# Optimization experiments

Measured on AMD Instinct MI355X. Metric: run time of the kernel, lower is better.

Reference implementation:

```python
import jax, jax.numpy as jnp
import numpy as np


def setup_inputs() -> dict:
    key = jax.random.key(0)
    k1, k2 = jax.random.split(key)
    querry_emb = jax.random.normal(k1, (4096, 1024), dtype=jnp.float32)
    traj_emb = jax.random.normal(k2, (8192, 1024), dtype=jnp.float32)
    return {"querry_emb": querry_emb, "traj_emb": traj_emb}


def reference(querry_emb, traj_emb):
    # Cosine-similarity score: (Q K^T) / (|q| outer |k|)  -> [Nq, Nk]
    q_norm = jnp.sqrt(jnp.sum(querry_emb * querry_emb, axis=1))  # [Nq]
    k_norm = jnp.sqrt(jnp.sum(traj_emb * traj_emb, axis=1))      # [Nk]
    score = jnp.einsum('qd,kd->qk', querry_emb, traj_emb) / (q_norm[:, None] * k_norm[None, :])
    # Softmax over key axis (torch dim=1 on [Nq, Nk])
    atten = jax.nn.softmax(score, axis=1)
    # Context: weighted sum of values (traj_emb)
    context = jnp.einsum('qk,kd->qd', atten, traj_emb)
    return context
```

## Files before the change

### kernel.cpp

```cpp
#include <hip/hip_runtime.h>

#define NQ 4096
#define NK 8192
#define DIM 1024

typedef __attribute__((ext_vector_type(8))) short short8;
typedef __attribute__((ext_vector_type(4))) float floatx4;
typedef unsigned int u32;
typedef __attribute__((address_space(3))) u32 lds_u32;
typedef __attribute__((address_space(1))) const u32 glb_u32;

__device__ __forceinline__ void gload_lds16(const void* g, void* l) {
    __builtin_amdgcn_global_load_lds((glb_u32*)g, (lds_u32*)l, 16, 0, 0);
}

__device__ __forceinline__ unsigned short f32_bf16(float f) {
    unsigned int u = __float_as_uint(f);
    u += 0x7fff + ((u >> 16) & 1);
    return (unsigned short)(u >> 16);
}

__global__ void prep_q_zero(const float* __restrict__ Q,
                            unsigned short* __restrict__ Qb,
                            float* __restrict__ inv_qn,
                            float* __restrict__ lsum,
                            float* __restrict__ out_zero) {
    int wave = threadIdx.x >> 6;
    int lane = threadIdx.x & 63;
    int row  = blockIdx.x * 4 + wave;
    const float* r = Q + (size_t)row * DIM;
    float s = 0.f;
#pragma unroll
    for (int c = 0; c < 4; ++c) {
        float4 f = *(const float4*)(r + c * 256 + lane * 4);
        s += f.x * f.x + f.y * f.y + f.z * f.z + f.w * f.w;
        ushort4 b;
        b.x = f32_bf16(f.x); b.y = f32_bf16(f.y);
        b.z = f32_bf16(f.z); b.w = f32_bf16(f.w);
        *(ushort4*)(Qb + (size_t)row * DIM + c * 256 + lane * 4) = b;
    }
#pragma unroll
    for (int off = 32; off > 0; off >>= 1) s += __shfl_xor(s, off);
    if (lane == 0) inv_qn[row] = 1.0f / sqrtf(s);

    float4 z = make_float4(0.f, 0.f, 0.f, 0.f);
    if (out_zero) {
#pragma unroll
        for (int c = 0; c < 4; ++c)
            *(float4*)(out_zero + (size_t)blockIdx.x * 4096 + c * 1024 + threadIdx.x * 4) = z;
    }
    if (blockIdx.x < 4)
        *(float4*)(lsum + blockIdx.x * 1024 + threadIdx.x * 4) = z;
}

__global__ void prep_norm_cvt(const float* __restrict__ src,
                              unsigned short* __restrict__ dst,
                              float* __restrict__ inv_norm) {
    int wave = threadIdx.x >> 6;
    int lane = threadIdx.x & 63;
    int row  = blockIdx.x * 4 + wave;
    const float* r = src + (size_t)row * DIM;
    float s = 0.f;
#pragma unroll
    for (int c = 0; c < 4; ++c) {
        float4 f = *(const float4*)(r + c * 256 + lane * 4);
        s += f.x * f.x + f.y * f.y + f.z * f.z + f.w * f.w;
        ushort4 b;
        b.x = f32_bf16(f.x); b.y = f32_bf16(f.y);
        b.z = f32_bf16(f.z); b.w = f32_bf16(f.w);
        *(ushort4*)(dst + (size_t)row * DIM + c * 256 + lane * 4) = b;
    }
#pragma unroll
    for (int off = 32; off > 0; off >>= 1) s += __shfl_xor(s, off);
    if (lane == 0) inv_norm[row] = 1.0f / sqrtf(s);
}

__global__ void transpose_cvt(const float* __restrict__ K,
                              unsigned short* __restrict__ Kt) {
    __shared__ float t[64][65];
    int kn0 = blockIdx.x * 64, d0 = blockIdx.y * 64;
    int tid = threadIdx.x;
    int r  = tid >> 4;
    int c4 = (tid & 15) * 4;
#pragma unroll
    for (int s = 0; s < 4; ++s) {
        int kk = s * 16 + r;
        float4 f = *(const float4*)(K + (size_t)(kn0 + kk) * DIM + d0 + c4);
        t[kk][c4 + 0] = f.x; t[kk][c4 + 1] = f.y;
        t[kk][c4 + 2] = f.z; t[kk][c4 + 3] = f.w;
    }
    __syncthreads();
#pragma unroll
    for (int s = 0; s < 4; ++s) {
        int dd = s * 16 + r;
        ushort4 b;
        b.x = f32_bf16(t[c4 + 0][dd]);
        b.y = f32_bf16(t[c4 + 1][dd]);
        b.z = f32_bf16(t[c4 + 2][dd]);
        b.w = f32_bf16(t[c4 + 3][dd]);
        *(ushort4*)(Kt + (size_t)(d0 + dd) * NK + kn0 + c4) = b;
    }
}

__global__ __launch_bounds__(512, 2) void score_gemm(
        const unsigned short* __restrict__ Qb,
        const unsigned short* __restrict__ Kb,
        const float* __restrict__ inv_qn,
        const float* __restrict__ inv_kn,
        unsigned short* __restrict__ P,
        float* __restrict__ lsum) {
    __shared__ __align__(16) unsigned short A_lds[2][2][256 * 32];
    __shared__ __align__(16) unsigned short B_lds[2][2][256 * 32];

    int bid = blockIdx.x;
    int swz = (bid & 7) * 64 + (bid >> 3);
    int q0  = (swz & 15) * 256;
    int n0  = (swz >> 4) * 256;

    int tid  = threadIdx.x;
    int wave = tid >> 6, lane = tid & 63;
    int wm = wave >> 2, wn = wave & 3;
    int quad = lane >> 4, l16 = lane & 15;
    int rcol = (quad ^ ((l16 >> 1) & 3)) * 8;

    int schunk = ((tid & 3) ^ ((tid >> 3) & 3)) * 8;
    const unsigned short* gA = Qb + (size_t)(q0 + (tid >> 2)) * DIM + schunk;
    const unsigned short* gB = Kb + (size_t)(n0 + (tid >> 2)) * DIM + schunk;

#define STG_A(t1, pan)                                                \
    do {                                                              \
        const unsigned short* _g = gA + (t1) * 64 + (pan) * 32;       \
        unsigned short* _l = &A_lds[(t1) & 1][pan][wave * 512];       \
        gload_lds16(_g, _l);                                          \
        gload_lds16(_g + (size_t)128 * DIM, _l + 4096);               \
    } while (0)
#define STG_B(t1, pan)                                                \
    do {                                                              \
        const unsigned short* _g = gB + (t1) * 64 + (pan) * 32;       \
        unsigned short* _l = &B_lds[(t1) & 1][pan][wave * 512];       \
        gload_lds16(_g, _l);                                          \
        gload_lds16(_g + (size_t)128 * DIM, _l + 4096);               \
    } while (0)

    floatx4 acc[8][4];
#pragma unroll
    for (int i = 0; i < 8; ++i)
#pragma unroll
        for (int j = 0; j < 4; ++j) acc[i][j] = (floatx4)(0.0f);

    short8 a[4][2], bA[2][2], bB[2][2];

    STG_A(0, 0); STG_A(0, 1); STG_B(0, 0); STG_B(0, 1);
    asm volatile("s_waitcnt vmcnt(0)" ::: "memory");
    __syncthreads();

    for (int t = 0; t < 16; ++t) {
        const unsigned short* A0 = &A_lds[t & 1][0][0];
        const unsigned short* A1 = &A_lds[t & 1][1][0];
        const unsigned short* B0 = &B_lds[t & 1][0][0];
        const unsigned short* B1 = &B_lds[t & 1][1][0];
        const int ar = (wm * 128 + l16) * 32 + rcol;
        const int br = (wn * 64 + l16) * 32 + rcol;

#pragma unroll
        for (int mi = 0; mi < 4; ++mi) {
            a[mi][0] = *(const short8*)&A0[ar + mi * 512];
            a[mi][1] = *(const short8*)&A1[ar + mi * 512];
        }
#pragma unroll
        for (int nj = 0; nj < 2; ++nj) {
            bA[nj][0] = *(const short8*)&B0[br + nj * 512];
            bA[nj][1] = *(const short8*)&B1[br + nj * 512];
        }
        if (t < 15) { STG_A(t + 1, 0); STG_A(t + 1, 1); }
        __builtin_amdgcn_s_barrier();
        __builtin_amdgcn_s_setprio(1);
#pragma unroll
        for (int mi = 0; mi < 4; ++mi)
#pragma unroll
            for (int nj = 0; nj < 2; ++nj) {
                acc[mi][nj] = __builtin_amdgcn_mfma_f32_16x16x32_bf16(bA[nj][0], a[mi][0], acc[mi][nj], 0, 0, 0);
                acc[mi][nj] = __builtin_amdgcn_mfma_f32_16x16x32_bf16(bA[nj][1], a[mi][1], acc[mi][nj], 0, 0, 0);
            }
        __builtin_amdgcn_s_setprio(0);
        __builtin_amdgcn_s_barrier();

#pragma unroll
        for (int nj = 0; nj < 2; ++nj) {
            bB[nj][0] = *(const short8*)&B0[br + 1024 + nj * 512];
            bB[nj][1] = *(const short8*)&B1[br + 1024 + nj * 512];
        }
        if (t < 15) { STG_B(t + 1, 0); STG_B(t + 1, 1); }
        __builtin_amdgcn_s_barrier();
        __builtin_amdgcn_s_setprio(1);
#pragma unroll
        for (int mi = 0; mi < 4; ++mi)
#pragma unroll
            for (int nj = 0; nj < 2; ++nj) {
                acc[mi][2 + nj] = __builtin_amdgcn_mfma_f32_16x16x32_bf16(bB[nj][0], a[mi][0], acc[mi][2 + nj], 0, 0, 0);
                acc[mi][2 + nj] = __builtin_amdgcn_mfma_f32_16x16x32_bf16(bB[nj][1], a[mi][1], acc[mi][2 + nj], 0, 0, 0);
            }
        __builtin_amdgcn_s_setprio(0);
        __builtin_amdgcn_s_barrier();

#pragma unroll
        for (int mi = 0; mi < 4; ++mi) {
            a[mi][0] = *(const short8*)&A0[ar + 2048 + mi * 512];
            a[mi][1] = *(const short8*)&A1[ar + 2048 + mi * 512];
        }
        __builtin_amdgcn_s_barrier();
        __builtin_amdgcn_s_setprio(1);
#pragma unroll
        for (int mi = 0; mi < 4; ++mi)
#pragma unroll
            for (int nj = 0; nj < 2; ++nj) {
                acc[4 + mi][2 + nj] = __builtin_amdgcn_mfma_f32_16x16x32_bf16(bB[nj][0], a[mi][0], acc[4 + mi][2 + nj], 0, 0, 0);
                acc[4 + mi][2 + nj] = __builtin_amdgcn_mfma_f32_16x16x32_bf16(bB[nj][1], a[mi][1], acc[4 + mi][2 + nj], 0, 0, 0);
            }
        __builtin_amdgcn_s_setprio(0);
        __builtin_amdgcn_s_barrier();

        __builtin_amdgcn_s_setprio(1);
#pragma unroll
        for (int mi = 0; mi < 4; ++mi)
#pragma unroll
            for (int nj = 0; nj < 2; ++nj) {
                acc[4 + mi][nj] = __builtin_amdgcn_mfma_f32_16x16x32_bf16(bA[nj][0], a[mi][0], acc[4 + mi][nj], 0, 0, 0);
                acc[4 + mi][nj] = __builtin_amdgcn_mfma_f32_16x16x32_bf16(bA[nj][1], a[mi][1], acc[4 + mi][nj], 0, 0, 0);
            }
        __builtin_amdgcn_s_setprio(0);
        if (t < 15) asm volatile("s_waitcnt vmcnt(0)" ::: "memory");
        __builtin_amdgcn_s_barrier();
    }
#undef STG_A
#undef STG_B

#pragma unroll
    for (int i = 0; i < 8; ++i) {
        int qrow = q0 + wm * 128 + i * 16 + l16;
        float iqn = inv_qn[qrow];
        float rs = 0.f;
#pragma unroll
        for (int j = 0; j < 4; ++j) {
            int ncol = n0 + wn * 64 + j * 16 + quad * 4;
            float4 ik = *(const float4*)&inv_kn[ncol];
            float p0 = __expf(acc[i][j][0] * iqn * ik.x);
            float p1 = __expf(acc[i][j][1] * iqn * ik.y);
            float p2 = __expf(acc[i][j][2] * iqn * ik.z);
            float p3 = __expf(acc[i][j][3] * iqn * ik.w);
            ushort4 pb;
            pb.x = f32_bf16(p0); pb.y = f32_bf16(p1);
            pb.z = f32_bf16(p2); pb.w = f32_bf16(p3);
            *(ushort4*)&P[(size_t)qrow * NK + ncol] = pb;
            rs += p0 + p1 + p2 + p3;
        }
        rs += __shfl_xor(rs, 16);
        rs += __shfl_xor(rs, 32);
        if (quad == 0) atomicAdd(&lsum[qrow], rs);
    }
}

__global__ void ctx_gemm_st(const unsigned short* __restrict__ P,
                            const unsigned short* __restrict__ Kt,
                            float* __restrict__ part) {
    __shared__ __align__(16) unsigned short As[128 * 32];
    __shared__ __align__(16) unsigned short Bs[128 * 32];
    int id = blockIdx.x;
    int r8 = id & 7;
    int t  = id >> 3;
    int x  = t & 7;
    int g  = ((t >> 3) << 3) | r8;
    int y  = g & 31;
    int z  = g >> 5;
    int q0 = y * 128;
    int d0 = x * 128;
    int kbase = z * (NK / 4);

    int tid = threadIdx.x;
    int wave = tid >> 6, lane = tid & 63;
    int wm = wave >> 1, wn = wave & 1;
    int quad = lane >> 4, l16 = lane & 15;

    int srow   = wave * 32 + (lane >> 2);
    int schunk = (((lane & 3) ^ ((lane >> 3) & 3))) * 8;
    const unsigned short* gA0 = P + (size_t)(q0 + srow) * NK + kbase + schunk;
    const unsigned short* gA1 = gA0 + (size_t)16 * NK;
    const unsigned short* gB0 = Kt + (size_t)(d0 + srow) * NK + kbase + schunk;
    const unsigned short* gB1 = gB0 + (size_t)16 * NK;
    unsigned short* lA0 = As + wave * 32 * 32;
    unsigned short* lA1 = lA0 + 16 * 32;
    unsigned short* lB0 = Bs + wave * 32 * 32;
    unsigned short* lB1 = lB0 + 16 * 32;

    int rcol = (quad ^ ((l16 >> 1) & 3)) * 8;

    floatx4 acc[4][4];
#pragma unroll
    for (int i = 0; i < 4; ++i)
#pragma unroll
        for (int j = 0; j < 4; ++j) acc[i][j] = (floatx4)(0.0f);

    for (int kb = 0; kb < (NK / 4) / 32; ++kb) {
        int k0 = kb * 32;
        __syncthreads();
        gload_lds16(gA0 + k0, lA0);
        gload_lds16(gA1 + k0, lA1);
        gload_lds16(gB0 + k0, lB0);
        gload_lds16(gB1 + k0, lB1);
        __syncthreads();
        short8 a[4], b[4];
#pragma unroll
        for (int i = 0; i < 4; ++i)
            a[i] = *(const short8*)&As[(wm * 64 + i * 16 + l16) * 32 + rcol];
#pragma unroll
        for (int j = 0; j < 4; ++j)
            b[j] = *(const short8*)&Bs[(wn * 64 + j * 16 + l16) * 32 + rcol];
#pragma unroll
        for (int i = 0; i < 4; ++i)
#pragma unroll
            for (int j = 0; j < 4; ++j)
                acc[i][j] = __builtin_amdgcn_mfma_f32_16x16x32_bf16(b[j], a[i], acc[i][j], 0, 0, 0);
    }

    float* pslice = part + (size_t)z * NQ * DIM;
#pragma unroll
    for (int i = 0; i < 4; ++i) {
        int qrow = q0 + wm * 64 + i * 16 + l16;
#pragma unroll
        for (int j = 0; j < 4; ++j) {
            int dcol = d0 + wn * 64 + j * 16 + quad * 4;
            float4 v;
            v.x = acc[i][j][0]; v.y = acc[i][j][1];
            v.z = acc[i][j][2]; v.w = acc[i][j][3];
            *(float4*)&pslice[(size_t)qrow * DIM + dcol] = v;
        }
    }
}

__global__ void reduce_out(const float* __restrict__ part,
                           const float* __restrict__ lsum,
                           float* __restrict__ out) {
    size_t idx = ((size_t)blockIdx.x * 256 + threadIdx.x) * 4;
    int q = (int)(idx >> 10);
    float inv = 1.0f / lsum[q];
    const size_t S = (size_t)NQ * DIM;
    float4 s0 = *(const float4*)(part + idx);
    float4 s1 = *(const float4*)(part + S + idx);
    float4 s2 = *(const float4*)(part + 2 * S + idx);
    float4 s3 = *(const float4*)(part + 3 * S + idx);
    float4 o;
    o.x = (s0.x + s1.x + s2.x + s3.x) * inv;
    o.y = (s0.y + s1.y + s2.y + s3.y) * inv;
    o.z = (s0.z + s1.z + s2.z + s3.z) * inv;
    o.w = (s0.w + s1.w + s2.w + s3.w) * inv;
    *(float4*)(out + idx) = o;
}

__global__ void ctx_gemm(const unsigned short* __restrict__ P,
                         const unsigned short* __restrict__ Kt,
                         const float* __restrict__ lsum,
                         float* __restrict__ out) {
    __shared__ __align__(16) unsigned short As[128 * 32];
    __shared__ __align__(16) unsigned short Bs[128 * 32];
    int id = blockIdx.x;
    int r8 = id & 7;
    int t  = id >> 3;
    int x  = t & 7;
    int g  = ((t >> 3) << 3) | r8;
    int y  = g & 31;
    int z  = g >> 5;
    int q0 = y * 128;
    int d0 = x * 128;
    int kbase = z * (NK / 4);

    int tid = threadIdx.x;
    int wave = tid >> 6, lane = tid & 63;
    int wm = wave >> 1, wn = wave & 1;
    int quad = lane >> 4, l16 = lane & 15;

    int srow   = wave * 32 + (lane >> 2);
    int schunk = (((lane & 3) ^ ((lane >> 3) & 3))) * 8;
    const unsigned short* gA0 = P + (size_t)(q0 + srow) * NK + kbase + schunk;
    const unsigned short* gA1 = gA0 + (size_t)16 * NK;
    const unsigned short* gB0 = Kt + (size_t)(d0 + srow) * NK + kbase + schunk;
    const unsigned short* gB1 = gB0 + (size_t)16 * NK;
    unsigned short* lA0 = As + wave * 32 * 32;
    unsigned short* lA1 = lA0 + 16 * 32;
    unsigned short* lB0 = Bs + wave * 32 * 32;
    unsigned short* lB1 = lB0 + 16 * 32;

    int rcol = (quad ^ ((l16 >> 1) & 3)) * 8;

    floatx4 acc[4][4];
#pragma unroll
    for (int i = 0; i < 4; ++i)
#pragma unroll
        for (int j = 0; j < 4; ++j) acc[i][j] = (floatx4)(0.0f);

    for (int kb = 0; kb < (NK / 4) / 32; ++kb) {
        int k0 = kb * 32;
        __syncthreads();
        gload_lds16(gA0 + k0, lA0);
        gload_lds16(gA1 + k0, lA1);
        gload_lds16(gB0 + k0, lB0);
        gload_lds16(gB1 + k0, lB1);
        __syncthreads();
        short8 a[4], b[4];
#pragma unroll
        for (int i = 0; i < 4; ++i)
            a[i] = *(const short8*)&As[(wm * 64 + i * 16 + l16) * 32 + rcol];
#pragma unroll
        for (int j = 0; j < 4; ++j)
            b[j] = *(const short8*)&Bs[(wn * 64 + j * 16 + l16) * 32 + rcol];
#pragma unroll
        for (int i = 0; i < 4; ++i)
#pragma unroll
            for (int j = 0; j < 4; ++j)
                acc[i][j] = __builtin_amdgcn_mfma_f32_16x16x32_bf16(a[i], b[j], acc[i][j], 0, 0, 0);
    }

#pragma unroll
    for (int i = 0; i < 4; ++i) {
        float invl[4];
#pragma unroll
        for (int r = 0; r < 4; ++r)
            invl[r] = 1.0f / lsum[q0 + wm * 64 + i * 16 + quad * 4 + r];
#pragma unroll
        for (int j = 0; j < 4; ++j) {
#pragma unroll
            for (int r = 0; r < 4; ++r) {
                int qrow = q0 + wm * 64 + i * 16 + quad * 4 + r;
                int dcol = d0 + wn * 64 + j * 16 + l16;
                atomicAdd(&out[(size_t)qrow * DIM + dcol], acc[i][j][r] * invl[r]);
            }
        }
    }
}

__global__ void fused_fallback(const float* __restrict__ Q,
                               const float* __restrict__ K,
                               float* __restrict__ out) {
    int wave = threadIdx.x >> 6, lane = threadIdx.x & 63;
    int q0 = blockIdx.x * 16 + wave * 4;
    float qv[4][16], acc[4][16], iqn[4], ls[4];
#pragma unroll
    for (int r = 0; r < 4; ++r) {
        float s = 0.f;
#pragma unroll
        for (int c = 0; c < 4; ++c) {
            float4 f = *(const float4*)(Q + (size_t)(q0 + r) * DIM + c * 256 + lane * 4);
            qv[r][c * 4 + 0] = f.x; qv[r][c * 4 + 1] = f.y;
            qv[r][c * 4 + 2] = f.z; qv[r][c * 4 + 3] = f.w;
            s += f.x * f.x + f.y * f.y + f.z * f.z + f.w * f.w;
        }
#pragma unroll
        for (int off = 32; off > 0; off >>= 1) s += __shfl_xor(s, off);
        iqn[r] = 1.0f / sqrtf(s);
        ls[r] = 0.f;
#pragma unroll
        for (int t = 0; t < 16; ++t) acc[r][t] = 0.f;
    }
    for (int k = 0; k < NK; ++k) {
        const float* kr = K + (size_t)k * DIM;
        float kv[16], ss = 0.f;
#pragma unroll
        for (int c = 0; c < 4; ++c) {
            float4 f = *(const float4*)(kr + c * 256 + lane * 4);
            kv[c * 4 + 0] = f.x; kv[c * 4 + 1] = f.y;
            kv[c * 4 + 2] = f.z; kv[c * 4 + 3] = f.w;
            ss += f.x * f.x + f.y * f.y + f.z * f.z + f.w * f.w;
        }
        float d0 = 0.f, d1 = 0.f, d2 = 0.f, d3 = 0.f;
#pragma unroll
        for (int t = 0; t < 16; ++t) {
            d0 += qv[0][t] * kv[t]; d1 += qv[1][t] * kv[t];
            d2 += qv[2][t] * kv[t]; d3 += qv[3][t] * kv[t];
        }
#pragma unroll
        for (int off = 32; off > 0; off >>= 1) {
            ss += __shfl_xor(ss, off);
            d0 += __shfl_xor(d0, off); d1 += __shfl_xor(d1, off);
            d2 += __shfl_xor(d2, off); d3 += __shfl_xor(d3, off);
        }
        float ikn = 1.0f / sqrtf(ss);
        float p0 = __expf(d0 * iqn[0] * ikn), p1 = __expf(d1 * iqn[1] * ikn);
        float p2 = __expf(d2 * iqn[2] * ikn), p3 = __expf(d3 * iqn[3] * ikn);
        ls[0] += p0; ls[1] += p1; ls[2] += p2; ls[3] += p3;
#pragma unroll
        for (int t = 0; t < 16; ++t) {
            acc[0][t] += p0 * kv[t]; acc[1][t] += p1 * kv[t];
            acc[2][t] += p2 * kv[t]; acc[3][t] += p3 * kv[t];
        }
    }
#pragma unroll
    for (int r = 0; r < 4; ++r) {
        float inv = 1.0f / ls[r];
#pragma unroll
        for (int c = 0; c < 4; ++c) {
            float4 o;
            o.x = acc[r][c * 4 + 0] * inv; o.y = acc[r][c * 4 + 1] * inv;
            o.z = acc[r][c * 4 + 2] * inv; o.w = acc[r][c * 4 + 3] * inv;
            *(float4*)(out + (size_t)(q0 + r) * DIM + c * 256 + lane * 4) = o;
        }
    }
}

extern "C" void kernel_launch(void* const* d_in, const int* in_sizes, int n_in,
                              void* d_out, int out_size, void* d_ws, size_t ws_size,
                              hipStream_t stream) {
    const float* Q = (const float*)d_in[0];
    const float* K = (const float*)d_in[1];
    float* out = (float*)d_out;
    char* ws = (char*)d_ws;

    const size_t REQ_T1 = ((size_t)152u << 20) + 65536;
    const size_t REQ_T2 = ((size_t)88u << 20) + 65536;

    if (ws_size >= REQ_T1) {
        unsigned short* Kt = (unsigned short*)(ws);
        unsigned short* Qb = (unsigned short*)(ws);
        unsigned short* Kb = (unsigned short*)(ws + (size_t)(8u << 20));
        unsigned short* P  = (unsigned short*)(ws + (size_t)(24u << 20));
        float* part   = (float*)(ws + (size_t)(88u << 20));
        float* inv_qn = (float*)(ws + (size_t)(152u << 20));
        float* inv_kn = (float*)(ws + (size_t)(152u << 20) + 16384);
        float* lsum   = (float*)(ws + (size_t)(152u << 20) + 49152);

        prep_q_zero<<<NQ / 4, 256, 0, stream>>>(Q, Qb, inv_qn, lsum, nullptr);
        prep_norm_cvt<<<NK / 4, 256, 0, stream>>>(K, Kb, inv_kn);
        score_gemm<<<512, 512, 0, stream>>>(Qb, Kb, inv_qn, inv_kn, P, lsum);
        transpose_cvt<<<dim3(NK / 64, DIM / 64), 256, 0, stream>>>(K, Kt);
        ctx_gemm_st<<<1024, 256, 0, stream>>>(P, Kt, part);
        reduce_out<<<NQ * DIM / 1024, 256, 0, stream>>>(part, lsum, out);
    } else if (ws_size >= REQ_T2) {
        unsigned short* Kt = (unsigned short*)(ws);
        unsigned short* Qb = (unsigned short*)(ws);
        unsigned short* Kb = (unsigned short*)(ws + (size_t)(8u << 20));
        unsigned short* P  = (unsigned short*)(ws + (size_t)(24u << 20));
        float* inv_qn = (float*)(ws + (size_t)(88u << 20));
        float* inv_kn = (float*)(ws + (size_t)(88u << 20) + 16384);
        float* lsum   = (float*)(ws + (size_t)(88u << 20) + 49152);

        prep_q_zero<<<NQ / 4, 256, 0, stream>>>(Q, Qb, inv_qn, lsum, out);
        prep_norm_cvt<<<NK / 4, 256, 0, stream>>>(K, Kb, inv_kn);
        score_gemm<<<512, 512, 0, stream>>>(Qb, Kb, inv_qn, inv_kn, P, lsum);
        transpose_cvt<<<dim3(NK / 64, DIM / 64), 256, 0, stream>>>(K, Kt);
        ctx_gemm<<<1024, 256, 0, stream>>>(P, Kt, lsum, out);
    } else {
        fused_fallback<<<NQ / 16, 256, 0, stream>>>(Q, K, out);
    }
}
```

Baseline: 280.7 us.

## Rewrite context GEMM with 256x256 tiles, double-buffered LDS and phased MFMA schedule

The split-K context GEMM moves from 128x128 tiles with 4 waves and a single-buffered 32-wide k step to 256x256 tiles with 8 waves, a 64-wide k step, and double-buffered LDS. The next tile is prefetched while the current one is computed. The MFMA work is split into four sub-phases with barriers and s_setprio so LDS reads, global loads and matrix ops interleave. The goal is more data reuse per loaded byte and less time stalled on global-to-LDS latency, at the cost of 128 KB of LDS, many more accumulator registers, and only 256 blocks in the grid.

```diff
diff --git a/kernel.cpp b/kernel.cpp
--- a/kernel.cpp
+++ b/kernel.cpp
@@ -260,72 +260,145 @@
     }
 }
 
-__global__ void ctx_gemm_st(const unsigned short* __restrict__ P,
-                            const unsigned short* __restrict__ Kt,
-                            float* __restrict__ part) {
-    __shared__ __align__(16) unsigned short As[128 * 32];
-    __shared__ __align__(16) unsigned short Bs[128 * 32];
-    int id = blockIdx.x;
-    int r8 = id & 7;
-    int t  = id >> 3;
-    int x  = t & 7;
-    int g  = ((t >> 3) << 3) | r8;
-    int y  = g & 31;
-    int z  = g >> 5;
-    int q0 = y * 128;
-    int d0 = x * 128;
+__global__ __launch_bounds__(512, 2) void ctx_gemm_st(
+        const unsigned short* __restrict__ P,
+        const unsigned short* __restrict__ Kt,
+        float* __restrict__ part) {
+    __shared__ __align__(16) unsigned short A_lds[2][2][256 * 32];
+    __shared__ __align__(16) unsigned short B_lds[2][2][256 * 32];
+
+    int bid = blockIdx.x;
+    int swz = (bid & 7) * 32 + (bid >> 3);
+    int z  = swz >> 6;
+    int y  = (swz >> 2) & 15;
+    int x  = swz & 3;
+    int q0 = y * 256;
+    int d0 = x * 256;
     int kbase = z * (NK / 4);
 
-    int tid = threadIdx.x;
+    int tid  = threadIdx.x;
     int wave = tid >> 6, lane = tid & 63;
-    int wm = wave >> 1, wn = wave & 1;
+    int wm = wave >> 2, wn = wave & 3;
     int quad = lane >> 4, l16 = lane & 15;
-
-    int srow   = wave * 32 + (lane >> 2);
-    int schunk = (((lane & 3) ^ ((lane >> 3) & 3))) * 8;
-    const unsigned short* gA0 = P + (size_t)(q0 + srow) * NK + kbase + schunk;
-    const unsigned short* gA1 = gA0 + (size_t)16 * NK;
-    const unsigned short* gB0 = Kt + (size_t)(d0 + srow) * NK + kbase + schunk;
-    const unsigned short* gB1 = gB0 + (size_t)16 * NK;
-    unsigned short* lA0 = As + wave * 32 * 32;
-    unsigned short* lA1 = lA0 + 16 * 32;
-    unsigned short* lB0 = Bs + wave * 32 * 32;
-    unsigned short* lB1 = lB0 + 16 * 32;
-
     int rcol = (quad ^ ((l16 >> 1) & 3)) * 8;
 
-    floatx4 acc[4][4];
-#pragma unroll
-    for (int i = 0; i < 4; ++i)
+    int schunk = ((tid & 3) ^ ((tid >> 3) & 3)) * 8;
+    const unsigned short* gA = P  + (size_t)(q0 + (tid >> 2)) * NK + kbase + schunk;
+    const unsigned short* gB = Kt + (size_t)(d0 + (tid >> 2)) * NK + kbase + schunk;
+
+#define STG_A(t1, pan)                                                \
+    do {                                                              \
+        const unsigned short* _g = gA + (t1) * 64 + (pan) * 32;       \
+        unsigned short* _l = &A_lds[(t1) & 1][pan][wave * 512];       \
+        gload_lds16(_g, _l);                                          \
+        gload_lds16(_g + (size_t)128 * NK, _l + 4096);                \
+    } while (0)
+#define STG_B(t1, pan)                                                \
+    do {                                                              \
+        const unsigned short* _g = gB + (t1) * 64 + (pan) * 32;       \
+        unsigned short* _l = &B_lds[(t1) & 1][pan][wave * 512];       \
+        gload_lds16(_g, _l);                                          \
+        gload_lds16(_g + (size_t)128 * NK, _l + 4096);                \
+    } while (0)
+
+    floatx4 acc[8][4];
+#pragma unroll
+    for (int i = 0; i < 8; ++i)
 #pragma unroll
         for (int j = 0; j < 4; ++j) acc[i][j] = (floatx4)(0.0f);
 
-    for (int kb = 0; kb < (NK / 4) / 32; ++kb) {
-        int k0 = kb * 32;
-        __syncthreads();
-        gload_lds16(gA0 + k0, lA0);
-        gload_lds16(gA1 + k0, lA1);
-        gload_lds16(gB0 + k0, lB0);
-        gload_lds16(gB1 + k0, lB1);
-        __syncthreads();
-        short8 a[4], b[4];
-#pragma unroll
-        for (int i = 0; i < 4; ++i)
-            a[i] = *(const short8*)&As[(wm * 64 + i * 16 + l16) * 32 + rcol];
-#pragma unroll
-        for (int j = 0; j < 4; ++j)
-            b[j] = *(const short8*)&Bs[(wn * 64 + j * 16 + l16) * 32 + rcol];
-#pragma unroll
-        for (int i = 0; i < 4; ++i)
-#pragma unroll
-            for (int j = 0; j < 4; ++j)
-                acc[i][j] = __builtin_amdgcn_mfma_f32_16x16x32_bf16(b[j], a[i], acc[i][j], 0, 0, 0);
-    }
+    short8 a[4][2], bA[2][2], bB[2][2];
+
+    STG_A(0, 0); STG_A(0, 1); STG_B(0, 0); STG_B(0, 1);
+    asm volatile("s_waitcnt vmcnt(0)" ::: "memory");
+    __syncthreads();
+
+    const int NT = (NK / 4) / 64;
+    for (int t = 0; t < NT; ++t) {
+        const unsigned short* A0 = &A_lds[t & 1][0][0];
+        const unsigned short* A1 = &A_lds[t & 1][1][0];
+        const unsigned short* B0 = &B_lds[t & 1][0][0];
+        const unsigned short* B1 = &B_lds[t & 1][1][0];
+        const int ar = (wm * 128 + l16) * 32 + rcol;
+        const int br = (wn * 64 + l16) * 32 + rcol;
+
+#pragma unroll
+        for (int mi = 0; mi < 4; ++mi) {
+            a[mi][0] = *(const short8*)&A0[ar + mi * 512];
+            a[mi][1] = *(const short8*)&A1[ar + mi * 512];
+        }
+#pragma unroll
+        for (int nj = 0; nj < 2; ++nj) {
+            bA[nj][0] = *(const short8*)&B0[br + nj * 512];
+            bA[nj][1] = *(const short8*)&B1[br + nj * 512];
+        }
+        if (t < NT - 1) { STG_A(t + 1, 0); STG_A(t + 1, 1); }
+        __builtin_amdgcn_s_barrier();
+        __builtin_amdgcn_s_setprio(1);
+#pragma unroll
+        for (int mi = 0; mi < 4; ++mi)
+#pragma unroll
+            for (int nj = 0; nj < 2; ++nj) {
+                acc[mi][nj] = __builtin_amdgcn_mfma_f32_16x16x32_bf16(bA[nj][0], a[mi][0], acc[mi][nj], 0, 0, 0);
+                acc[mi][nj] = __builtin_amdgcn_mfma_f32_16x16x32_bf16(bA[nj][1], a[mi][1], acc[mi][nj], 0, 0, 0);
+            }
+        __builtin_amdgcn_s_setprio(0);
+        __builtin_amdgcn_s_barrier();
+
+#pragma unroll
+        for (int nj = 0; nj < 2; ++nj) {
+            bB[nj][0] = *(const short8*)&B0[br + 1024 + nj * 512];
+            bB[nj][1] = *(const short8*)&B1[br + 1024 + nj * 512];
+        }
+        if (t < NT - 1) { STG_B(t + 1, 0); STG_B(t + 1, 1); }
+        __builtin_amdgcn_s_barrier();
+        __builtin_amdgcn_s_setprio(1);
+#pragma unroll
+        for (int mi = 0; mi < 4; ++mi)
+#pragma unroll
+            for (int nj = 0; nj < 2; ++nj) {
+                acc[mi][2 + nj] = __builtin_amdgcn_mfma_f32_16x16x32_bf16(bB[nj][0], a[mi][0], acc[mi][2 + nj], 0, 0, 0);
+                acc[mi][2 + nj] = __builtin_amdgcn_mfma_f32_16x16x32_bf16(bB[nj][1], a[mi][1], acc[mi][2 + nj], 0, 0, 0);
+            }
+        __builtin_amdgcn_s_setprio(0);
+        __builtin_amdgcn_s_barrier();
+
+#pragma unroll
+        for (int mi = 0; mi < 4; ++mi) {
+            a[mi][0] = *(const short8*)&A0[ar + 2048 + mi * 512];
+            a[mi][1] = *(const short8*)&A1[ar + 2048 + mi * 512];
+        }
+        __builtin_amdgcn_s_barrier();
+        __builtin_amdgcn_s_setprio(1);
+#pragma unroll
+        for (int mi = 0; mi < 4; ++mi)
+#pragma unroll
+            for (int nj = 0; nj < 2; ++nj) {
+                acc[4 + mi][2 + nj] = __builtin_amdgcn_mfma_f32_16x16x32_bf16(bB[nj][0], a[mi][0], acc[4 + mi][2 + nj], 0, 0, 0);
+                acc[4 + mi][2 + nj] = __builtin_amdgcn_mfma_f32_16x16x32_bf16(bB[nj][1], a[mi][1], acc[4 + mi][2 + nj], 0, 0, 0);
+            }
+        __builtin_amdgcn_s_setprio(0);
+        __builtin_amdgcn_s_barrier();
+
+        __builtin_amdgcn_s_setprio(1);
+#pragma unroll
+        for (int mi = 0; mi < 4; ++mi)
+#pragma unroll
+            for (int nj = 0; nj < 2; ++nj) {
+                acc[4 + mi][nj] = __builtin_amdgcn_mfma_f32_16x16x32_bf16(bA[nj][0], a[mi][0], acc[4 + mi][nj], 0, 0, 0);
+                acc[4 + mi][nj] = __builtin_amdgcn_mfma_f32_16x16x32_bf16(bA[nj][1], a[mi][1], acc[4 + mi][nj], 0, 0, 0);
+            }
+        __builtin_amdgcn_s_setprio(0);
+        if (t < NT - 1) asm volatile("s_waitcnt vmcnt(0)" ::: "memory");
+        __builtin_amdgcn_s_barrier();
+    }
+#undef STG_A
+#undef STG_B
 
     float* pslice = part + (size_t)z * NQ * DIM;
 #pragma unroll
-    for (int i = 0; i < 4; ++i) {
-        int qrow = q0 + wm * 64 + i * 16 + l16;
+    for (int i = 0; i < 8; ++i) {
+        int qrow = q0 + wm * 128 + i * 16 + l16;
 #pragma unroll
         for (int j = 0; j < 4; ++j) {
             int dcol = d0 + wn * 64 + j * 16 + quad * 4;
@@ -530,7 +603,7 @@
         prep_norm_cvt<<<NK / 4, 256, 0, stream>>>(K, Kb, inv_kn);
         score_gemm<<<512, 512, 0, stream>>>(Qb, Kb, inv_qn, inv_kn, P, lsum);
         transpose_cvt<<<dim3(NK / 64, DIM / 64), 256, 0, stream>>>(K, Kt);
-        ctx_gemm_st<<<1024, 256, 0, stream>>>(P, Kt, part);
+        ctx_gemm_st<<<256, 512, 0, stream>>>(P, Kt, part);
         reduce_out<<<NQ * DIM / 1024, 256, 0, stream>>>(part, lsum, out);
     } else if (ws_size >= REQ_T2) {
         unsigned short* Kt = (unsigned short*)(ws);
```

Measured after the change: 261.3 us. 1.07x faster.

## Use 4-stage LDS pipeline in score GEMM and enlarge ctx GEMM tiles

Applied to the files above, without the earlier changes.

The score GEMM drops its double-buffered, split-panel schedule for a 4-deep ring of 32-wide K tiles. Loads are issued three tiles ahead and gated with vmcnt waits, so each iteration needs one barrier instead of several. The split-K context GEMM is rebuilt on the same 256x256-tile, 512-thread pipelined body in place of its synchronous 128x128 loop. This cuts launched blocks from 1024 to 256 and raises data reuse per block, but uses more LDS and registers per block and leaves fewer blocks to spread across CUs.

```diff
diff --git a/kernel.cpp b/kernel.cpp
--- a/kernel.cpp
+++ b/kernel.cpp
@@ -18,6 +18,36 @@
     unsigned int u = __float_as_uint(f);
     u += 0x7fff + ((u >> 16) & 1);
     return (unsigned short)(u >> 16);
+}
+
+__device__ __forceinline__ void tile_body(const unsigned short* A0,
+                                          const unsigned short* B0,
+                                          int ar, int br,
+                                          floatx4 (&acc)[8][4]) {
+    short8 a[4], b[4];
+#pragma unroll
+    for (int nj = 0; nj < 4; ++nj)
+        b[nj] = *(const short8*)&B0[br + nj * 512];
+#pragma unroll
+    for (int mi = 0; mi < 4; ++mi)
+        a[mi] = *(const short8*)&A0[ar + mi * 512];
+    __builtin_amdgcn_s_setprio(1);
+#pragma unroll
+    for (int mi = 0; mi < 4; ++mi)
+#pragma unroll
+        for (int nj = 0; nj < 4; ++nj)
+            acc[mi][nj] = __builtin_amdgcn_mfma_f32_16x16x32_bf16(b[nj], a[mi], acc[mi][nj], 0, 0, 0);
+    __builtin_amdgcn_s_setprio(0);
+#pragma unroll
+    for (int mi = 0; mi < 4; ++mi)
+        a[mi] = *(const short8*)&A0[ar + 2048 + mi * 512];
+    __builtin_amdgcn_s_setprio(1);
+#pragma unroll
+    for (int mi = 0; mi < 4; ++mi)
+#pragma unroll
+        for (int nj = 0; nj < 4; ++nj)
+            acc[4 + mi][nj] = __builtin_amdgcn_mfma_f32_16x16x32_bf16(b[nj], a[mi], acc[4 + mi][nj], 0, 0, 0);
+    __builtin_amdgcn_s_setprio(0);
 }
 
 __global__ void prep_q_zero(const float* __restrict__ Q,
@@ -109,8 +139,8 @@
         const float* __restrict__ inv_kn,
         unsigned short* __restrict__ P,
         float* __restrict__ lsum) {
-    __shared__ __align__(16) unsigned short A_lds[2][2][256 * 32];
-    __shared__ __align__(16) unsigned short B_lds[2][2][256 * 32];
+    __shared__ __align__(16) unsigned short A_lds[4][256 * 32];
+    __shared__ __align__(16) unsigned short B_lds[4][256 * 32];
 
     int bid = blockIdx.x;
     int swz = (bid & 7) * 64 + (bid >> 3);
@@ -127,20 +157,17 @@
     const unsigned short* gA = Qb + (size_t)(q0 + (tid >> 2)) * DIM + schunk;
     const unsigned short* gB = Kb + (size_t)(n0 + (tid >> 2)) * DIM + schunk;
 
-#define STG_A(t1, pan)                                                \
+#define STG(t1)                                                       \
     do {                                                              \
-        const unsigned short* _g = gA + (t1) * 64 + (pan) * 32;       \
-        unsigned short* _l = &A_lds[(t1) & 1][pan][wave * 512];       \
-        gload_lds16(_g, _l);                                          \
-        gload_lds16(_g + (size_t)128 * DIM, _l + 4096);               \
+        const unsigned short* _ga = gA + (t1) * 32;                   \
+        const unsigned short* _gb = gB + (t1) * 32;                   \
+        unsigned short* _la = &A_lds[(t1) & 3][wave * 512];           \
+        unsigned short* _lb = &B_lds[(t1) & 3][wave * 512];           \
+        gload_lds16(_ga, _la);                                        \
+        gload_lds16(_ga + (size_t)128 * DIM, _la + 4096);             \
+        gload_lds16(_gb, _lb);                                        \
+        gload_lds16(_gb + (size_t)128 * DIM, _lb + 4096);             \
     } while (0)
-#define STG_B(t1, pan)                                                \
-    do {                                                              \
-        const unsigned short* _g = gB + (t1) * 64 + (pan) * 32;       \
-        unsigned short* _l = &B_lds[(t1) & 1][pan][wave * 512];       \
-        gload_lds16(_g, _l);                                          \
-        gload_lds16(_g + (size_t)128 * DIM, _l + 4096);               \
-    } while (0)
 
     floatx4 acc[8][4];
 #pragma unroll
@@ -148,92 +175,32 @@
 #pragma unroll
         for (int j = 0; j < 4; ++j) acc[i][j] = (floatx4)(0.0f);
 
-    short8 a[4][2], bA[2][2], bB[2][2];
-
-    STG_A(0, 0); STG_A(0, 1); STG_B(0, 0); STG_B(0, 1);
+    const int ar = (wm * 128 + l16) * 32 + rcol;
+    const int br = (wn * 64 + l16) * 32 + rcol;
+
+    STG(0); STG(1); STG(2);
+
+#pragma unroll 4
+    for (int t = 0; t < 28; ++t) {
+        asm volatile("s_waitcnt vmcnt(8)" ::: "memory");
+        __builtin_amdgcn_s_barrier();
+        STG(t + 3);
+        tile_body(&A_lds[t & 3][0], &B_lds[t & 3][0], ar, br, acc);
+    }
+    asm volatile("s_waitcnt vmcnt(8)" ::: "memory");
+    __builtin_amdgcn_s_barrier();
+    STG(31);
+    tile_body(&A_lds[0][0], &B_lds[0][0], ar, br, acc);
+    asm volatile("s_waitcnt vmcnt(8)" ::: "memory");
+    __builtin_amdgcn_s_barrier();
+    tile_body(&A_lds[1][0], &B_lds[1][0], ar, br, acc);
+    asm volatile("s_waitcnt vmcnt(4)" ::: "memory");
+    __builtin_amdgcn_s_barrier();
+    tile_body(&A_lds[2][0], &B_lds[2][0], ar, br, acc);
     asm volatile("s_waitcnt vmcnt(0)" ::: "memory");
-    __syncthreads();
-
-    for (int t = 0; t < 16; ++t) {
-        const unsigned short* A0 = &A_lds[t & 1][0][0];
-        const unsigned short* A1 = &A_lds[t & 1][1][0];
-        const unsigned short* B0 = &B_lds[t & 1][0][0];
-        const unsigned short* B1 = &B_lds[t & 1][1][0];
-        const int ar = (wm * 128 + l16) * 32 + rcol;
-        const int br = (wn * 64 + l16) * 32 + rcol;
-
-#pragma unroll
-        for (int mi = 0; mi < 4; ++mi) {
-            a[mi][0] = *(const short8*)&A0[ar + mi * 512];
-            a[mi][1] = *(const short8*)&A1[ar + mi * 512];
-        }
-#pragma unroll
-        for (int nj = 0; nj < 2; ++nj) {
-            bA[nj][0] = *(const short8*)&B0[br + nj * 512];
-            bA[nj][1] = *(const short8*)&B1[br + nj * 512];
-        }
-        if (t < 15) { STG_A(t + 1, 0); STG_A(t + 1, 1); }
-        __builtin_amdgcn_s_barrier();
-        __builtin_amdgcn_s_setprio(1);
-#pragma unroll
-        for (int mi = 0; mi < 4; ++mi)
-#pragma unroll
-            for (int nj = 0; nj < 2; ++nj) {
-                acc[mi][nj] = __builtin_amdgcn_mfma_f32_16x16x32_bf16(bA[nj][0], a[mi][0], acc[mi][nj], 0, 0, 0);
-                acc[mi][nj] = __builtin_amdgcn_mfma_f32_16x16x32_bf16(bA[nj][1], a[mi][1], acc[mi][nj], 0, 0, 0);
-            }
-        __builtin_amdgcn_s_setprio(0);
-        __builtin_amdgcn_s_barrier();
-
-#pragma unroll
-        for (int nj = 0; nj < 2; ++nj) {
-            bB[nj][0] = *(const short8*)&B0[br + 1024 + nj * 512];
-            bB[nj][1] = *(const short8*)&B1[br + 1024 + nj * 512];
-        }
-        if (t < 15) { STG_B(t + 1, 0); STG_B(t + 1, 1); }
-        __builtin_amdgcn_s_barrier();
-        __builtin_amdgcn_s_setprio(1);
-#pragma unroll
-        for (int mi = 0; mi < 4; ++mi)
-#pragma unroll
-            for (int nj = 0; nj < 2; ++nj) {
-                acc[mi][2 + nj] = __builtin_amdgcn_mfma_f32_16x16x32_bf16(bB[nj][0], a[mi][0], acc[mi][2 + nj], 0, 0, 0);
-                acc[mi][2 + nj] = __builtin_amdgcn_mfma_f32_16x16x32_bf16(bB[nj][1], a[mi][1], acc[mi][2 + nj], 0, 0, 0);
-            }
-        __builtin_amdgcn_s_setprio(0);
-        __builtin_amdgcn_s_barrier();
-
-#pragma unroll
-        for (int mi = 0; mi < 4; ++mi) {
-            a[mi][0] = *(const short8*)&A0[ar + 2048 + mi * 512];
-            a[mi][1] = *(const short8*)&A1[ar + 2048 + mi * 512];
-        }
-        __builtin_amdgcn_s_barrier();
-        __builtin_amdgcn_s_setprio(1);
-#pragma unroll
-        for (int mi = 0; mi < 4; ++mi)
-#pragma unroll
-            for (int nj = 0; nj < 2; ++nj) {
-                acc[4 + mi][2 + nj] = __builtin_amdgcn_mfma_f32_16x16x32_bf16(bB[nj][0], a[mi][0], acc[4 + mi][2 + nj], 0, 0, 0);
-                acc[4 + mi][2 + nj] = __builtin_amdgcn_mfma_f32_16x16x32_bf16(bB[nj][1], a[mi][1], acc[4 + mi][2 + nj], 0, 0, 0);
-            }
-        __builtin_amdgcn_s_setprio(0);
-        __builtin_amdgcn_s_barrier();
-
-        __builtin_amdgcn_s_setprio(1);
-#pragma unroll
-        for (int mi = 0; mi < 4; ++mi)
-#pragma unroll
-            for (int nj = 0; nj < 2; ++nj) {
-                acc[4 + mi][nj] = __builtin_amdgcn_mfma_f32_16x16x32_bf16(bA[nj][0], a[mi][0], acc[4 + mi][nj], 0, 0, 0);
-                acc[4 + mi][nj] = __builtin_amdgcn_mfma_f32_16x16x32_bf16(bA[nj][1], a[mi][1], acc[4 + mi][nj], 0, 0, 0);
-            }
-        __builtin_amdgcn_s_setprio(0);
-        if (t < 15) asm volatile("s_waitcnt vmcnt(0)" ::: "memory");
-        __builtin_amdgcn_s_barrier();
-    }
-#undef STG_A
-#undef STG_B
+    __builtin_amdgcn_s_barrier();
+    tile_body(&A_lds[3][0], &B_lds[3][0], ar, br, acc);
+#undef STG
 
 #pragma unroll
     for (int i = 0; i < 8; ++i) {
@@ -260,72 +227,81 @@
     }
 }
 
-__global__ void ctx_gemm_st(const unsigned short* __restrict__ P,
-                            const unsigned short* __restrict__ Kt,
-                            float* __restrict__ part) {
-    __shared__ __align__(16) unsigned short As[128 * 32];
-    __shared__ __align__(16) unsigned short Bs[128 * 32];
-    int id = blockIdx.x;
-    int r8 = id & 7;
-    int t  = id >> 3;
-    int x  = t & 7;
-    int g  = ((t >> 3) << 3) | r8;
-    int y  = g & 31;
-    int z  = g >> 5;
-    int q0 = y * 128;
-    int d0 = x * 128;
+__global__ __launch_bounds__(512, 2) void ctx_gemm_st(
+        const unsigned short* __restrict__ P,
+        const unsigned short* __restrict__ Kt,
+        float* __restrict__ part) {
+    __shared__ __align__(16) unsigned short A_lds[4][256 * 32];
+    __shared__ __align__(16) unsigned short B_lds[4][256 * 32];
+
+    int bid = blockIdx.x;
+    int swz = (bid & 7) * 32 + (bid >> 3);
+    int z  = swz >> 6;
+    int y  = (swz >> 2) & 15;
+    int x  = swz & 3;
+    int q0 = y * 256;
+    int d0 = x * 256;
     int kbase = z * (NK / 4);
 
-    int tid = threadIdx.x;
+    int tid  = threadIdx.x;
     int wave = tid >> 6, lane = tid & 63;
-    int wm = wave >> 1, wn = wave & 1;
+    int wm = wave >> 2, wn = wave & 3;
     int quad = lane >> 4, l16 = lane & 15;
-
-    int srow   = wave * 32 + (lane >> 2);
-    int schunk = (((lane & 3) ^ ((lane >> 3) & 3))) * 8;
-    const unsigned short* gA0 = P + (size_t)(q0 + srow) * NK + kbase + schunk;
-    const unsigned short* gA1 = gA0 + (size_t)16 * NK;
-    const unsigned short* gB0 = Kt + (size_t)(d0 + srow) * NK + kbase + schunk;
-    const unsigned short* gB1 = gB0 + (size_t)16 * NK;
-    unsigned short* lA0 = As + wave * 32 * 32;
-    unsigned short* lA1 = lA0 + 16 * 32;
-    unsigned short* lB0 = Bs + wave * 32 * 32;
-    unsigned short* lB1 = lB0 + 16 * 32;
-
     int rcol = (quad ^ ((l16 >> 1) & 3)) * 8;
 
-    floatx4 acc[4][4];
-#pragma unroll
-    for (int i = 0; i < 4; ++i)
+    int schunk = ((tid & 3) ^ ((tid >> 3) & 3)) * 8;
+    const unsigned short* gA = P  + (size_t)(q0 + (tid >> 2)) * NK + kbase + schunk;
+    const unsigned short* gB = Kt + (size_t)(d0 + (tid >> 2)) * NK + kbase + schunk;
+
+#define STG(t1)                                                       \
+    do {                                                              \
+        const unsigned short* _ga = gA + (t1) * 32;                   \
+        const unsigned short* _gb = gB + (t1) * 32;                   \
+        unsigned short* _la = &A_lds[(t1) & 3][wave * 512];           \
+        unsigned short* _lb = &B_lds[(t1) & 3][wave * 512];           \
+        gload_lds16(_ga, _la);                                        \
+        gload_lds16(_ga + (size_t)128 * NK, _la + 4096);              \
+        gload_lds16(_gb, _lb);                                        \
+        gload_lds16(_gb + (size_t)128 * NK, _lb + 4096);              \
+    } while (0)
+
+    floatx4 acc[8][4];
+#pragma unroll
+    for (int i = 0; i < 8; ++i)
 #pragma unroll
         for (int j = 0; j < 4; ++j) acc[i][j] = (floatx4)(0.0f);
 
-    for (int kb = 0; kb < (NK / 4) / 32; ++kb) {
-        int k0 = kb * 32;
-        __syncthreads();
-        gload_lds16(gA0 + k0, lA0);
-        gload_lds16(gA1 + k0, lA1);
-        gload_lds16(gB0 + k0, lB0);
-        gload_lds16(gB1 + k0, lB1);
-        __syncthreads();
-        short8 a[4], b[4];
-#pragma unroll
-        for (int i = 0; i < 4; ++i)
-            a[i] = *(const short8*)&As[(wm * 64 + i * 16 + l16) * 32 + rcol];
-#pragma unroll
-        for (int j = 0; j < 4; ++j)
-            b[j] = *(const short8*)&Bs[(wn * 64 + j * 16 + l16) * 32 + rcol];
-#pragma unroll
-        for (int i = 0; i < 4; ++i)
-#pragma unroll
-            for (int j = 0; j < 4; ++j)
-                acc[i][j] = __builtin_amdgcn_mfma_f32_16x16x32_bf16(b[j], a[i], acc[i][j], 0, 0, 0);
-    }
+    const int ar = (wm * 128 + l16) * 32 + rcol;
+    const int br = (wn * 64 + l16) * 32 + rcol;
+
+    STG(0); STG(1); STG(2);
+
+#pragma unroll 4
+    for (int t = 0; t < 60; ++t) {
+        asm volatile("s_waitcnt vmcnt(8)" ::: "memory");
+        __builtin_amdgcn_s_barrier();
+        STG(t + 3);
+        tile_body(&A_lds[t & 3][0], &B_lds[t & 3][0], ar, br, acc);
+    }
+    asm volatile("s_waitcnt vmcnt(8)" ::: "memory");
+    __builtin_amdgcn_s_barrier();
+    STG(63);
+    tile_body(&A_lds[0][0], &B_lds[0][0], ar, br, acc);
+    asm volatile("s_waitcnt vmcnt(8)" ::: "memory");
+    __builtin_amdgcn_s_barrier();
+    tile_body(&A_lds[1][0], &B_lds[1][0], ar, br, acc);
+    asm volatile("s_waitcnt vmcnt(4)" ::: "memory");
+    __builtin_amdgcn_s_barrier();
+    tile_body(&A_lds[2][0], &B_lds[2][0], ar, br, acc);
+    asm volatile("s_waitcnt vmcnt(0)" ::: "memory");
+    __builtin_amdgcn_s_barrier();
+    tile_body(&A_lds[3][0], &B_lds[3][0], ar, br, acc);
+#undef STG
 
     float* pslice = part + (size_t)z * NQ * DIM;
 #pragma unroll
-    for (int i = 0; i < 4; ++i) {
-        int qrow = q0 + wm * 64 + i * 16 + l16;
+    for (int i = 0; i < 8; ++i) {
+        int qrow = q0 + wm * 128 + i * 16 + l16;
 #pragma unroll
         for (int j = 0; j < 4; ++j) {
             int dcol = d0 + wn * 64 + j * 16 + quad * 4;
@@ -530,7 +506,7 @@
         prep_norm_cvt<<<NK / 4, 256, 0, stream>>>(K, Kb, inv_kn);
         score_gemm<<<512, 512, 0, stream>>>(Qb, Kb, inv_qn, inv_kn, P, lsum);
         transpose_cvt<<<dim3(NK / 64, DIM / 64), 256, 0, stream>>>(K, Kt);
-        ctx_gemm_st<<<1024, 256, 0, stream>>>(P, Kt, part);
+        ctx_gemm_st<<<256, 512, 0, stream>>>(P, Kt, part);
         reduce_out<<<NQ * DIM / 1024, 256, 0, stream>>>(part, lsum, out);
     } else if (ws_size >= REQ_T2) {
         unsigned short* Kt = (unsigned short*)(ws);
```

Result: faster. 263.7 us (-6.0%).
